# Optimization experiments

Hardware: AMD Instinct MI355X
Metric: run time of the kernel (lower is better)

Reference implementation:

```python
import jax, jax.numpy as jnp
import numpy as np

TEMPERATURE = 0.3
MEAN_REDUCTION = False


def setup_inputs() -> dict:
    key = jax.random.key(0)
    k1, k2 = jax.random.split(key)
    N, D = 8192, 256
    features = jax.random.normal(k1, (N, D), dtype=jnp.float32)
    labels = jax.random.randint(k2, (N,), 0, 10, dtype=jnp.int64)
    return {"features": features, "labels": labels}


def reference(features, labels):
    # L2-normalize rows (torch F.normalize, eps=1e-12)
    norm = jnp.maximum(jnp.linalg.norm(features, axis=1, keepdims=True), 1e-12)
    f = features / norm
    N = f.shape[0]
    # Full Gram matrix of cosine similarities scaled by temperature: [N, N]
    S = jnp.matmul(f, f.T) / TEMPERATURE
    not_self = ~jnp.eye(N, dtype=bool)
    same_label = (labels[:, None] == labels[None, :]) & not_self  # positives mask
    pos_cnt = jnp.sum(same_label, axis=1)  # [N]
    # log of denominator: log sum_{j != i} exp(S_ij), stable
    log_denom = jax.scipy.special.logsumexp(jnp.where(not_self, S, -jnp.inf), axis=1)
    # mean over positives of log(exp(S_ij)/denom) = mean(S_ij) - log_denom
    mean_pos = jnp.sum(jnp.where(same_label, S, 0.0), axis=1) / jnp.maximum(pos_cnt, 1)
    loss_i = mean_pos - log_denom  # [N]
    valid = pos_cnt > 0  # rows with no positives are skipped in original loop
    loss = -jnp.sum(jnp.where(valid, loss_i, 0.0))
    if MEAN_REDUCTION:
        loss = loss / jnp.sum(valid).astype(loss.dtype)
    return loss
```

## Files before the change

### kernel.cpp

```cpp
#include <hip/hip_runtime.h>

typedef __bf16 v8bf __attribute__((ext_vector_type(8)));
typedef float v4f __attribute__((ext_vector_type(4)));
typedef unsigned int v4u __attribute__((ext_vector_type(4)));

static constexpr int NR = 8192;
static constexpr int DD = 256;
static constexpr float INV_T = 1.0f / 0.3f;

static constexpr size_t FBF_OFF = 0;
static constexpr size_t SE_OFF  = 4194304;
static constexpr size_t G_OFF   = SE_OFF + 8192 * 4;
static constexpr size_t CNT_OFF = G_OFF + 2560 * 4;

__global__ __launch_bounds__(256) void k_zero(float* se, float* g, int* cnt, float* out) {
    const int i = blockIdx.x * 256 + threadIdx.x;
    for (int idx = i; idx < 8192; idx += gridDim.x * 256) se[idx] = 0.f;
    for (int idx = i; idx < 2560; idx += gridDim.x * 256) g[idx] = 0.f;
    if (i < 16) cnt[i] = 0;
    if (i == 0) out[0] = 0.f;
}

__global__ __launch_bounds__(256) void k_norm(const float* __restrict__ x,
                                              const int* __restrict__ lab,
                                              unsigned short* __restrict__ fbf,
                                              float* __restrict__ g,
                                              int* __restrict__ cnt) {
    __shared__ float gsh[2560];
    __shared__ int csh[16];
    const int tid = threadIdx.x;
    const int w = tid >> 6, l = tid & 63;
    for (int i = tid; i < 2560; i += 256) gsh[i] = 0.f;
    if (tid < 16) csh[tid] = 0;
    __syncthreads();
    #pragma unroll
    for (int it = 0; it < 8; ++it) {
        const int row = blockIdx.x * 32 + it * 4 + w;
        const float4 v = *reinterpret_cast<const float4*>(x + row * DD + l * 4);
        float ss = v.x * v.x + v.y * v.y + v.z * v.z + v.w * v.w;
        #pragma unroll
        for (int m = 1; m < 64; m <<= 1) ss += __shfl_xor(ss, m, 64);
        const float rn = 1.0f / fmaxf(sqrtf(ss), 1e-12f);
        const float f0 = v.x * rn, f1 = v.y * rn, f2 = v.z * rn, f3 = v.w * rn;
        union { __bf16 h[4]; uint2 u; } pk;
        pk.h[0] = (__bf16)f0; pk.h[1] = (__bf16)f1;
        pk.h[2] = (__bf16)f2; pk.h[3] = (__bf16)f3;
        *reinterpret_cast<uint2*>(fbf + row * DD + l * 4) = pk.u;
        const int lb = lab[row];
        float* gb = &gsh[lb * DD + l * 4];
        atomicAdd(gb + 0, f0); atomicAdd(gb + 1, f1);
        atomicAdd(gb + 2, f2); atomicAdd(gb + 3, f3);
        if (l == 0) atomicAdd(&csh[lb], 1);
    }
    __syncthreads();
    for (int i = tid; i < 2560; i += 256) atomicAdd(&g[i], gsh[i]);
    if (tid < 10) atomicAdd(&cnt[tid], csh[tid]);
}

__global__ __launch_bounds__(256, 2) void k_score(const unsigned short* __restrict__ fbf,
                                                  float* __restrict__ sumexp) {
    __shared__ unsigned short Bsh[2][32 * 256];
    const int tid = threadIdx.x;
    const int w = tid >> 6, l = tid & 63;
    const int ll = l & 15, lh = l >> 4;
    const int rb = blockIdx.x & 31;
    const int cc = blockIdx.x >> 5;
    const int row0 = rb * 256 + w * 64;
    const int c0 = cc * 512;
    const char* fbase = (const char*)fbf;

    v4u a[4][8];
    #pragma unroll
    for (int mr = 0; mr < 4; ++mr) {
        const char* rp = fbase + (size_t)(row0 + mr * 16 + ll) * 512 + lh * 16;
        #pragma unroll
        for (int ks = 0; ks < 8; ++ks) {
            a[mr][ks] = *reinterpret_cast<const v4u*>(rp + ks * 64);
            asm volatile("" : "+v"(a[mr][ks]));
        }
    }

    float se[4][4];
    #pragma unroll
    for (int mr = 0; mr < 4; ++mr)
        #pragma unroll
        for (int r = 0; r < 4; ++r) se[mr][r] = 0.f;

    const unsigned wbase = (unsigned)w * 4096u;
    char* lds0 = (char*)&Bsh[0][0];
    char* lds1 = (char*)&Bsh[1][0];

    auto stage = [&](int buf, int s) {
        char* lb = buf ? lds1 : lds0;
        #pragma unroll
        for (int t = 0; t < 4; ++t) {
            const unsigned o   = wbase + t * 1024u + (unsigned)l * 16u;
            const unsigned col = o >> 9;
            const unsigned kb  = o & 511u;
            const unsigned src = kb ^ ((col & 7u) << 4);
            const char* gp = fbase + (size_t)(c0 + s * 32 + (int)col) * 512 + src;
            __builtin_amdgcn_global_load_lds(
                (const __attribute__((address_space(1))) void*)gp,
                (__attribute__((address_space(3))) void*)(lb + wbase + t * 1024u),
                16, 0, 0);
        }
    };

    stage(0, 0);
    __syncthreads();

    for (int s = 0; s < 16; ++s) {
        if (s < 15) stage((s + 1) & 1, s + 1);
        const char* lb = (s & 1) ? lds1 : lds0;
        v4f acc[4][2];
        #pragma unroll
        for (int mr = 0; mr < 4; ++mr) {
            acc[mr][0] = (v4f){0.f, 0.f, 0.f, 0.f};
            acc[mr][1] = (v4f){0.f, 0.f, 0.f, 0.f};
        }
        #pragma unroll
        for (int ks = 0; ks < 8; ++ks) {
            const unsigned kb = (unsigned)(ks * 64 + lh * 16);
            const unsigned ad = (unsigned)ll * 512u + (kb ^ (((unsigned)ll & 7u) << 4));
            const v8bf b0 = *reinterpret_cast<const v8bf*>(lb + ad);
            const v8bf b1 = *reinterpret_cast<const v8bf*>(lb + ad + 8192);
            #pragma unroll
            for (int mr = 0; mr < 4; ++mr) {
                const v8bf av = __builtin_bit_cast(v8bf, a[mr][ks]);
                acc[mr][0] = __builtin_amdgcn_mfma_f32_16x16x32_bf16(av, b0, acc[mr][0], 0, 0, 0);
                acc[mr][1] = __builtin_amdgcn_mfma_f32_16x16x32_bf16(av, b1, acc[mr][1], 0, 0, 0);
            }
        }
        #pragma unroll
        for (int mr = 0; mr < 4; ++mr)
            #pragma unroll
            for (int nr = 0; nr < 2; ++nr)
                #pragma unroll
                for (int r = 0; r < 4; ++r)
                    se[mr][r] += __expf(acc[mr][nr][r] * INV_T);
        __syncthreads();
    }

    #pragma unroll
    for (int mr = 0; mr < 4; ++mr)
        #pragma unroll
        for (int r = 0; r < 4; ++r) {
            float v = se[mr][r];
            v += __shfl_xor(v, 1, 64);
            v += __shfl_xor(v, 2, 64);
            v += __shfl_xor(v, 4, 64);
            v += __shfl_xor(v, 8, 64);
            if (ll == 0)
                atomicAdd(&sumexp[row0 + mr * 16 + lh * 4 + r], v);
        }
}

__global__ __launch_bounds__(256) void k_final(const unsigned short* __restrict__ fbf,
                                               const float* __restrict__ sumexp,
                                               const float* __restrict__ g,
                                               const int* __restrict__ cnt,
                                               const int* __restrict__ lab,
                                               float* __restrict__ out) {
    __shared__ float lsum[16];
    const int tid = threadIdx.x;
    const int grp = tid >> 4, gl = tid & 15;
    const int row = blockIdx.x * 16 + grp;
    const int lb = lab[row];
    const char* rp = (const char*)fbf + (size_t)row * 512 + gl * 32;
    const uint4 u0 = *reinterpret_cast<const uint4*>(rp);
    const uint4 u1 = *reinterpret_cast<const uint4*>(rp + 16);
    const float* gp = g + lb * 256 + gl * 16;
    const float4 g0 = *reinterpret_cast<const float4*>(gp + 0);
    const float4 g1 = *reinterpret_cast<const float4*>(gp + 4);
    const float4 g2 = *reinterpret_cast<const float4*>(gp + 8);
    const float4 g3 = *reinterpret_cast<const float4*>(gp + 12);
    float d = 0.f;
    auto dot8 = [&](const uint4& u, const float4& a, const float4& b) {
        d += __uint_as_float(u.x << 16) * a.x + __uint_as_float(u.x & 0xffff0000u) * a.y
           + __uint_as_float(u.y << 16) * a.z + __uint_as_float(u.y & 0xffff0000u) * a.w
           + __uint_as_float(u.z << 16) * b.x + __uint_as_float(u.z & 0xffff0000u) * b.y
           + __uint_as_float(u.w << 16) * b.z + __uint_as_float(u.w & 0xffff0000u) * b.w;
    };
    dot8(u0, g0, g1);
    dot8(u1, g2, g3);
    d += __shfl_xor(d, 1, 64);
    d += __shfl_xor(d, 2, 64);
    d += __shfl_xor(d, 4, 64);
    d += __shfl_xor(d, 8, 64);
    if (gl == 0) {
        const int pc = cnt[lb] - 1;
        const float mp = (d - 1.0f) * INV_T / (float)(pc > 1 ? pc : 1);
        const float denom = sumexp[row] - __expf(INV_T);
        lsum[grp] = (pc > 0) ? (logf(denom) - mp) : 0.f;
    }
    __syncthreads();
    if (tid == 0) {
        float s = 0.f;
        #pragma unroll
        for (int i = 0; i < 16; ++i) s += lsum[i];
        atomicAdd(out, s);
    }
}

extern "C" void kernel_launch(void* const* d_in, const int* in_sizes, int n_in,
                              void* d_out, int out_size, void* d_ws, size_t ws_size,
                              hipStream_t stream) {
    const float* feat = (const float*)d_in[0];
    const int* labels = (const int*)d_in[1];
    float* out = (float*)d_out;
    char* ws = (char*)d_ws;
    unsigned short* fbf = (unsigned short*)(ws + FBF_OFF);
    float* se = (float*)(ws + SE_OFF);
    float* g  = (float*)(ws + G_OFF);
    int* cnt  = (int*)(ws + CNT_OFF);

    k_zero<<<dim3(8), dim3(256), 0, stream>>>(se, g, cnt, out);
    k_norm<<<dim3(256), dim3(256), 0, stream>>>(feat, labels, fbf, g, cnt);
    k_score<<<dim3(512), dim3(256), 0, stream>>>(fbf, se);
    k_final<<<dim3(512), dim3(256), 0, stream>>>(fbf, se, g, cnt, labels, out);
}
```

Before: 80.70 us.

## Load B tiles directly from global into registers, dropping LDS staging

The score kernel stops staging B column tiles through double-buffered shared memory with async global-to-LDS loads and barriers. Each wave now reads its own B fragments straight from global memory into registers every iteration, so there is no LDS and no __syncthreads. This removes barrier and LDS traffic, but the four waves in a block now each re-read the same B data from global/L2, and the loads are no longer prefetched ahead of the MFMAs, so load latency may be exposed.

```diff
diff --git a/kernel.cpp b/kernel.cpp
--- a/kernel.cpp
+++ b/kernel.cpp
@@ -59,7 +59,6 @@
 
 __global__ __launch_bounds__(256, 2) void k_score(const unsigned short* __restrict__ fbf,
                                                   float* __restrict__ sumexp) {
-    __shared__ unsigned short Bsh[2][32 * 256];
     const int tid = threadIdx.x;
     const int w = tid >> 6, l = tid & 63;
     const int ll = l & 15, lh = l >> 4;
@@ -86,32 +85,17 @@
         #pragma unroll
         for (int r = 0; r < 4; ++r) se[mr][r] = 0.f;
 
-    const unsigned wbase = (unsigned)w * 4096u;
-    char* lds0 = (char*)&Bsh[0][0];
-    char* lds1 = (char*)&Bsh[1][0];
-
-    auto stage = [&](int buf, int s) {
-        char* lb = buf ? lds1 : lds0;
-        #pragma unroll
-        for (int t = 0; t < 4; ++t) {
-            const unsigned o   = wbase + t * 1024u + (unsigned)l * 16u;
-            const unsigned col = o >> 9;
-            const unsigned kb  = o & 511u;
-            const unsigned src = kb ^ ((col & 7u) << 4);
-            const char* gp = fbase + (size_t)(c0 + s * 32 + (int)col) * 512 + src;
-            __builtin_amdgcn_global_load_lds(
-                (const __attribute__((address_space(1))) void*)gp,
-                (__attribute__((address_space(3))) void*)(lb + wbase + t * 1024u),
-                16, 0, 0);
-        }
-    };
-
-    stage(0, 0);
-    __syncthreads();
-
+    const char* bp0 = fbase + (size_t)(c0 + ll) * 512 + lh * 16;
+    const char* bp1 = fbase + (size_t)(c0 + 16 + ll) * 512 + lh * 16;
+
+    #pragma unroll 1
     for (int s = 0; s < 16; ++s) {
-        if (s < 15) stage((s + 1) & 1, s + 1);
-        const char* lb = (s & 1) ? lds1 : lds0;
+        v4u b0[8], b1[8];
+        #pragma unroll
+        for (int ks = 0; ks < 8; ++ks) {
+            b0[ks] = *reinterpret_cast<const v4u*>(bp0 + ks * 64);
+            b1[ks] = *reinterpret_cast<const v4u*>(bp1 + ks * 64);
+        }
         v4f acc[4][2];
         #pragma unroll
         for (int mr = 0; mr < 4; ++mr) {
@@ -120,15 +104,13 @@
         }
         #pragma unroll
         for (int ks = 0; ks < 8; ++ks) {
-            const unsigned kb = (unsigned)(ks * 64 + lh * 16);
-            const unsigned ad = (unsigned)ll * 512u + (kb ^ (((unsigned)ll & 7u) << 4));
-            const v8bf b0 = *reinterpret_cast<const v8bf*>(lb + ad);
-            const v8bf b1 = *reinterpret_cast<const v8bf*>(lb + ad + 8192);
+            const v8bf vb0 = __builtin_bit_cast(v8bf, b0[ks]);
+            const v8bf vb1 = __builtin_bit_cast(v8bf, b1[ks]);
             #pragma unroll
             for (int mr = 0; mr < 4; ++mr) {
                 const v8bf av = __builtin_bit_cast(v8bf, a[mr][ks]);
-                acc[mr][0] = __builtin_amdgcn_mfma_f32_16x16x32_bf16(av, b0, acc[mr][0], 0, 0, 0);
-                acc[mr][1] = __builtin_amdgcn_mfma_f32_16x16x32_bf16(av, b1, acc[mr][1], 0, 0, 0);
+                acc[mr][0] = __builtin_amdgcn_mfma_f32_16x16x32_bf16(av, vb0, acc[mr][0], 0, 0, 0);
+                acc[mr][1] = __builtin_amdgcn_mfma_f32_16x16x32_bf16(av, vb1, acc[mr][1], 0, 0, 0);
             }
         }
         #pragma unroll
@@ -138,7 +120,8 @@
                 #pragma unroll
                 for (int r = 0; r < 4; ++r)
                     se[mr][r] += __expf(acc[mr][nr][r] * INV_T);
-        __syncthreads();
+        bp0 += 32 * 512;
+        bp1 += 32 * 512;
     }
 
     #pragma unroll
```

Result: slower. 113.9 us (+41.1%).

## Exploit Gram matrix symmetry: compute upper-triangular tiles and scatter column sums

Applied to the files above, without the earlier changes.

Since S is symmetric, the score kernel now visits only upper-triangular 256x256 tile pairs (528 blocks) instead of the full matrix. Off-diagonal blocks also accumulate per-column exp sums in shared memory and add them to the column rows' sum-of-exp, which roughly halves the MFMA and exp work. The double-buffer sync is also reworked to use explicit vmcnt waits and raw barriers. The costs are extra shuffles and LDS atomics per step, more global atomics, and a serial loop at block start to decode the tile index.

```diff
diff --git a/kernel.cpp b/kernel.cpp
--- a/kernel.cpp
+++ b/kernel.cpp
@@ -60,14 +60,21 @@
 __global__ __launch_bounds__(256, 2) void k_score(const unsigned short* __restrict__ fbf,
                                                   float* __restrict__ sumexp) {
     __shared__ unsigned short Bsh[2][32 * 256];
+    __shared__ float colsum[256];
     const int tid = threadIdx.x;
     const int w = tid >> 6, l = tid & 63;
     const int ll = l & 15, lh = l >> 4;
-    const int rb = blockIdx.x & 31;
-    const int cc = blockIdx.x >> 5;
+
+    int bid = blockIdx.x, rb = 0;
+    while (bid >= 32 - rb) { bid -= 32 - rb; ++rb; }
+    const int cb = rb + bid;
+    const bool offdiag = (rb != cb);
+
     const int row0 = rb * 256 + w * 64;
-    const int c0 = cc * 512;
+    const int c0 = cb * 256;
     const char* fbase = (const char*)fbf;
+
+    colsum[tid] = 0.f;
 
     v4u a[4][8];
     #pragma unroll
@@ -107,10 +114,17 @@
     };
 
     stage(0, 0);
-    __syncthreads();
-
-    for (int s = 0; s < 16; ++s) {
-        if (s < 15) stage((s + 1) & 1, s + 1);
+
+    #pragma unroll 1
+    for (int s = 0; s < 8; ++s) {
+        if (s < 7) {
+            stage((s + 1) & 1, s + 1);
+            asm volatile("s_waitcnt vmcnt(4)" ::: "memory");
+        } else {
+            asm volatile("s_waitcnt vmcnt(0)" ::: "memory");
+        }
+        __builtin_amdgcn_s_barrier();
+
         const char* lb = (s & 1) ? lds1 : lds0;
         v4f acc[4][2];
         #pragma unroll
@@ -131,14 +145,26 @@
                 acc[mr][1] = __builtin_amdgcn_mfma_f32_16x16x32_bf16(av, b1, acc[mr][1], 0, 0, 0);
             }
         }
+        float cp0 = 0.f, cp1 = 0.f;
         #pragma unroll
         for (int mr = 0; mr < 4; ++mr)
             #pragma unroll
-            for (int nr = 0; nr < 2; ++nr)
-                #pragma unroll
-                for (int r = 0; r < 4; ++r)
-                    se[mr][r] += __expf(acc[mr][nr][r] * INV_T);
-        __syncthreads();
+            for (int r = 0; r < 4; ++r) {
+                const float e0 = __expf(acc[mr][0][r] * INV_T);
+                const float e1 = __expf(acc[mr][1][r] * INV_T);
+                se[mr][r] += e0 + e1;
+                cp0 += e0; cp1 += e1;
+            }
+        if (offdiag) {
+            cp0 += __shfl_xor(cp0, 16, 64); cp0 += __shfl_xor(cp0, 32, 64);
+            cp1 += __shfl_xor(cp1, 16, 64); cp1 += __shfl_xor(cp1, 32, 64);
+            if (lh == 0) {
+                atomicAdd(&colsum[s * 32 + ll], cp0);
+                atomicAdd(&colsum[s * 32 + 16 + ll], cp1);
+            }
+        }
+        asm volatile("s_waitcnt lgkmcnt(0)" ::: "memory");
+        __builtin_amdgcn_s_barrier();
     }
 
     #pragma unroll
@@ -153,6 +179,10 @@
             if (ll == 0)
                 atomicAdd(&sumexp[row0 + mr * 16 + lh * 4 + r], v);
         }
+
+    if (offdiag) {
+        atomicAdd(&sumexp[c0 + tid], colsum[tid]);
+    }
 }
 
 __global__ __launch_bounds__(256) void k_final(const unsigned short* __restrict__ fbf,
@@ -216,6 +246,6 @@
 
     k_zero<<<dim3(8), dim3(256), 0, stream>>>(se, g, cnt, out);
     k_norm<<<dim3(256), dim3(256), 0, stream>>>(feat, labels, fbf, g, cnt);
-    k_score<<<dim3(512), dim3(256), 0, stream>>>(fbf, se);
+    k_score<<<dim3(528), dim3(256), 0, stream>>>(fbf, se);
     k_final<<<dim3(512), dim3(256), 0, stream>>>(fbf, se, g, cnt, labels, out);
 }
```

Result: slower. 86.01 us (+6.6%).
